# Kernel optimization log

Measured on AMD Instinct MI355X. Metric: run time of the kernel, lower is better.

The kernel has to match this reference:

```python
import jax, jax.numpy as jnp
import numpy as np

B, N, C = 8, 16384, 256
HEADS = 8
TOK = 4  # token_size = (4, 4)


def _unfold3(x):
    # x: (b, c, h, w) -> (b, c, 9, h, w); 3x3 neighborhood, zero padded.
    b, c, h, w = x.shape
    p = jnp.pad(x, ((0, 0), (0, 0), (1, 1), (1, 1)))
    pat = jnp.stack([p[:, :, 1 + dy:1 + dy + h, 1 + dx:1 + dx + w]
                     for dy in (-1, 0, 1) for dx in (-1, 0, 1)], axis=2)
    return pat


def _fold3(u):
    # u: (b, k, 9, h, w) -> (b, k, h, w); scatter-add inverse of _unfold3
    # (matches F.conv_transpose2d with eye(9) kernels, stride 1, pad 1).
    b, k, _, h, w = u.shape
    p = jnp.pad(u, ((0, 0), (0, 0), (0, 0), (1, 1), (1, 1)))
    out = jnp.zeros((b, k, h, w), u.dtype)
    i = 0
    for dy in (-1, 0, 1):
        for dx in (-1, 0, 1):
            out = out + p[:, :, i, 1 - dy:1 - dy + h, 1 - dx:1 - dx + w]
            i += 1
    return out


def setup_inputs() -> dict:
    key = jax.random.key(0)
    k1, k2, k3, k4 = jax.random.split(key, 4)
    x = jax.random.normal(k1, (B, N, C), jnp.float32)
    qkv_w = jax.random.normal(k2, (3 * C, C), jnp.float32) * 0.02
    proj_w = jax.random.normal(k3, (C, C), jnp.float32) * 0.02
    proj_b = jax.random.normal(k4, (C,), jnp.float32) * 0.02
    return {"x": x, "qkv_w": qkv_w, "proj_w": proj_w, "proj_b": proj_b}


def reference(x, qkv_w, proj_w, proj_b):
    b, n, c = x.shape
    H = W = int(np.sqrt(n))
    hh, ww = H // TOK, W // TOK
    nw = hh * ww                      # number of super tokens
    scale = c ** -0.5
    hd = c // HEADS
    head_scale = hd ** -0.5

    xi = jnp.transpose(x, (0, 2, 1)).reshape(b, c, H, W)
    blocks = xi.reshape(b, c, hh, TOK, ww, TOK)
    wf = blocks.mean(axis=(3, 5))                      # (b,c,hh,ww) adaptive avg pool
    pix = blocks.transpose(0, 2, 4, 3, 5, 1).reshape(b, nw, TOK * TOK, c)

    # 3x3 super-token neighborhood features: (b, nw, c, 9)
    wfu = _unfold3(wf).reshape(b, c, 9, nw).transpose(0, 3, 1, 2)

    # pixel <-> super-token affinity, softmax over 9 neighbors
    aff = jax.nn.softmax(jnp.einsum('bnpc,bnck->bnpk', pix, wfu) * scale, axis=-1)

    # normalization: fold of per-window affinity mass -> (b,1,hh,ww)
    aff_sum = _fold3(aff.sum(2).transpose(0, 2, 1).reshape(b, 1, 9, hh, ww))

    # aggregate pixels into super tokens and fold neighborhoods back
    wf2 = jnp.einsum('bnpc,bnpk->bnck', pix, aff)      # (b,nw,c,9)
    wf2 = _fold3(wf2.transpose(0, 2, 3, 1).reshape(b, c, 9, hh, ww))  # (b,c,hh,ww)
    wf2 = wf2 / (jax.lax.stop_gradient(aff_sum) + 1e-12)

    # inner attention over super tokens (non-SDPA: softmax over key axis)
    qkv = jnp.einsum('oc,bchw->bohw', qkv_w, wf2).reshape(b, HEADS, 3 * hd, nw)
    q, k, v = jnp.split(qkv, 3, axis=2)                # each (b,heads,hd,nw)
    attn = jnp.einsum('bhdn,bhdm->bhnm', k, q) * head_scale
    attn = jax.nn.softmax(attn, axis=-2)               # softmax over key index n
    ref = jnp.einsum('bhdn,bhnm->bhdm', v, attn).reshape(b, c, hh, ww)
    ref = jnp.einsum('oc,bchw->bohw', proj_w, ref) + proj_b[None, :, None, None]

    # scatter refined super tokens back to pixels through the affinity
    wfu2 = _unfold3(ref).reshape(b, c, 9, nw).transpose(0, 3, 1, 2)   # (b,nw,c,9)
    pix2 = jnp.einsum('bnck,bnpk->bncp', wfu2, aff)    # (b,nw,c,16)
    pix2 = pix2.reshape(b, hh, ww, c, TOK, TOK).transpose(0, 3, 1, 4, 2, 5)
    pix2 = pix2.reshape(b, c, H, W)
    # NOTE: torch does a raw memory reshape (B,C,H,W)->(B,H*W,C), not a transpose;
    # we replicate that exactly.
    return pix2.reshape(b, H * W, c)
```

## Files before the change

### kernel.cpp

```cpp
#include <hip/hip_runtime.h>

typedef short short8 __attribute__((ext_vector_type(8)));
typedef float f32x4 __attribute__((ext_vector_type(4)));

__device__ __forceinline__ unsigned short f2bf(float x) {
  union { float f; unsigned int u; } v; v.f = x;
  unsigned int r = (v.u + 0x7FFFu + ((v.u >> 16) & 1u)) >> 16;
  return (unsigned short)r;
}
__device__ __forceinline__ float bf2f(unsigned short u) {
  union { unsigned int u; float f; } v; v.u = ((unsigned int)u) << 16;
  return v.f;
}

__global__ __launch_bounds__(256) void k0_wconv(const float* __restrict__ qkvw,
                                                const float* __restrict__ projw,
                                                unsigned short* __restrict__ wqkvbf,
                                                unsigned short* __restrict__ wprojbf) {
  int i = blockIdx.x * 256 + threadIdx.x;
  if (i < 768 * 256) wqkvbf[i] = f2bf(qkvw[i]);
  if (i < 256 * 256) wprojbf[i] = f2bf(projw[i]);
}

__global__ __launch_bounds__(256) void k1_pool(const float* __restrict__ x,
                                               float* __restrict__ wf) {
  int t = threadIdx.x;
  int blk = blockIdx.x;
  int b = blk >> 10, pos = blk & 1023;
  int y = pos >> 5, xw = pos & 31;
  const float* xb = x + (size_t)b * 4194304;
  float acc = 0.f;
  #pragma unroll
  for (int p = 0; p < 16; ++p) {
    int h = 4 * y + (p >> 2), w = 4 * xw + (p & 3);
    acc += xb[(size_t)(h * 128 + w) * 256 + t];
  }
  wf[(size_t)blk * 256 + t] = acc * 0.0625f;
}

__global__ __launch_bounds__(256) void k2_winaff(const float* __restrict__ x,
                                                 const float* __restrict__ wf,
                                                 float* __restrict__ aff_g,
                                                 unsigned short* __restrict__ agg,
                                                 float* __restrict__ asum_w) {
  __shared__ float pixs[16][272];
  __shared__ float wfu[9][272];
  __shared__ float aff_s[16][12];
  int t = threadIdx.x;
  int blk = blockIdx.x;
  int b = blk >> 10, pos = blk & 1023;
  int y = pos >> 5, xw = pos & 31;
  const float* xb = x + (size_t)b * 4194304;

  #pragma unroll
  for (int p = 0; p < 16; ++p) {
    int h = 4 * y + (p >> 2), w = 4 * xw + (p & 3);
    pixs[p][t] = xb[(size_t)(h * 128 + w) * 256 + t];
  }
  #pragma unroll
  for (int i = 0; i < 9; ++i) {
    int dy = i / 3 - 1, dx = i % 3 - 1;
    int ny = y + dy, nx = xw + dx;
    float v = 0.f;
    if (ny >= 0 && ny < 32 && nx >= 0 && nx < 32)
      v = wf[((size_t)(b * 1024) + ny * 32 + nx) * 256 + t];
    wfu[i][t] = v;
  }
  __syncthreads();

  int pp = t >> 4, sub = t & 15;
  #pragma unroll
  for (int i = 0; i < 9; ++i) {
    float acc = 0.f;
    #pragma unroll
    for (int j = 0; j < 16; ++j) acc += pixs[pp][sub + 16 * j] * wfu[i][sub + 16 * j];
    acc += __shfl_xor(acc, 1);
    acc += __shfl_xor(acc, 2);
    acc += __shfl_xor(acc, 4);
    acc += __shfl_xor(acc, 8);
    if (sub == 0) aff_s[pp][i] = acc * 0.0625f;
  }
  __syncthreads();

  if (t < 16) {
    float m = aff_s[t][0];
    #pragma unroll
    for (int i = 1; i < 9; ++i) m = fmaxf(m, aff_s[t][i]);
    float e[9]; float s = 0.f;
    #pragma unroll
    for (int i = 0; i < 9; ++i) { e[i] = __expf(aff_s[t][i] - m); s += e[i]; }
    float inv = 1.f / s;
    #pragma unroll
    for (int i = 0; i < 9; ++i) aff_s[t][i] = e[i] * inv;
  }
  __syncthreads();

  if (t < 144) aff_g[(size_t)blk * 144 + t] = aff_s[t / 9][t % 9];
  if (t < 9) {
    float s = 0.f;
    #pragma unroll
    for (int p = 0; p < 16; ++p) s += aff_s[p][t];
    asum_w[blk * 9 + t] = s;
  }

  #pragma unroll
  for (int k = 0; k < 9; ++k) {
    float acc = 0.f;
    #pragma unroll
    for (int p = 0; p < 16; ++p) acc += pixs[p][t] * aff_s[p][k];
    agg[((size_t)blk * 9 + k) * 256 + t] = f2bf(acc);
  }
}

__global__ __launch_bounds__(256) void k3_gather(const unsigned short* __restrict__ agg,
                                                 const float* __restrict__ asum_w,
                                                 unsigned short* __restrict__ wf2bf) {
  int t = threadIdx.x;
  int blk = blockIdx.x;
  int b = blk >> 10, pos = blk & 1023;
  int y = pos >> 5, xw = pos & 31;
  float acc = 0.f, den = 0.f;
  #pragma unroll
  for (int i = 0; i < 9; ++i) {
    int dy = i / 3 - 1, dx = i % 3 - 1;
    int sy = y - dy, sx = xw - dx;
    if (sy < 0 || sy >= 32 || sx < 0 || sx >= 32) continue;
    size_t un = (size_t)(b * 1024) + sy * 32 + sx;
    acc += bf2f(agg[(un * 9 + i) * 256 + t]);
    den += asum_w[un * 9 + i];
  }
  wf2bf[(size_t)blk * 256 + t] = f2bf(acc / (den + 1e-12f));
}

__global__ __launch_bounds__(256) void k4_qkv(const unsigned short* __restrict__ wbf,
                                              const unsigned short* __restrict__ xbf,
                                              unsigned short* __restrict__ qt,
                                              unsigned short* __restrict__ kt,
                                              unsigned short* __restrict__ vt) {
  int tid = threadIdx.x, lane = tid & 63, wv = tid >> 6;
  int l15 = lane & 15, g = lane >> 4;
  int nb = blockIdx.x * 64 + (wv & 1) * 32;
  int ob = blockIdx.y * 64 + (wv >> 1) * 32;
  int b = blockIdx.z;
  const unsigned short* X = xbf + (size_t)b * 262144;
  f32x4 acc[2][2] = {};
  for (int cc = 0; cc < 256; cc += 32) {
    short8 af[2], bfr[2];
    #pragma unroll
    for (int oi = 0; oi < 2; ++oi)
      af[oi] = *(const short8*)(wbf + (size_t)(ob + oi * 16 + l15) * 256 + cc + g * 8);
    #pragma unroll
    for (int ni = 0; ni < 2; ++ni)
      bfr[ni] = *(const short8*)(X + (size_t)(nb + ni * 16 + l15) * 256 + cc + g * 8);
    #pragma unroll
    for (int oi = 0; oi < 2; ++oi)
      #pragma unroll
      for (int ni = 0; ni < 2; ++ni)
        acc[oi][ni] = __builtin_amdgcn_mfma_f32_16x16x32_bf16(af[oi], bfr[ni], acc[oi][ni], 0, 0, 0);
  }
  #pragma unroll
  for (int oi = 0; oi < 2; ++oi)
    #pragma unroll
    for (int ni = 0; ni < 2; ++ni)
      #pragma unroll
      for (int r = 0; r < 4; ++r) {
        int o = ob + oi * 16 + g * 4 + r;
        int n = nb + ni * 16 + l15;
        unsigned short bv = f2bf(acc[oi][ni][r]);
        int head = o / 96;
        int rr = o - head * 96;
        size_t bh = (size_t)(b * 8 + head);
        if (rr < 32) qt[(bh * 1024 + n) * 32 + rr] = bv;
        else if (rr < 64) kt[(bh * 1024 + n) * 32 + (rr - 32)] = bv;
        else vt[(bh * 32 + (rr - 64)) * 1024 + n] = bv;
      }
}

__global__ __launch_bounds__(256) void k5_attn(const unsigned short* __restrict__ qt,
                                               const unsigned short* __restrict__ kt,
                                               const unsigned short* __restrict__ vt,
                                               unsigned short* __restrict__ refpre) {
  __shared__ short P_lds[4][32][40];
  __shared__ float out_lds[4][32][33];
  __shared__ float den_lds[4][32];
  int tid = threadIdx.x, lane = tid & 63, wv = tid >> 6;
  int l15 = lane & 15, g = lane >> 4;
  int mt = blockIdx.x, h = blockIdx.y, b = blockIdx.z;
  const unsigned short* qtb = qt + ((size_t)(b * 8 + h) * 1024) * 32;
  const unsigned short* ktb = kt + ((size_t)(b * 8 + h) * 1024) * 32;
  const unsigned short* vtb = vt + ((size_t)(b * 8 + h) * 32) * 1024;

  short8 qf[2];
  #pragma unroll
  for (int mi = 0; mi < 2; ++mi) {
    int m = mt * 32 + mi * 16 + l15;
    qf[mi] = *(const short8*)(qtb + (size_t)m * 32 + g * 8);
  }
  f32x4 oacc[2][2] = {};
  float dsum0 = 0.f, dsum1 = 0.f;
  const float hs = 0.17677669529663687f;

  for (int c8 = 0; c8 < 8; ++c8) {
    int nchunk = wv * 256 + c8 * 32;
    f32x4 sf[2][2];
    #pragma unroll
    for (int nt = 0; nt < 2; ++nt) {
      int n = nchunk + nt * 16 + l15;
      short8 kf = *(const short8*)(ktb + (size_t)n * 32 + g * 8);
      #pragma unroll
      for (int mi = 0; mi < 2; ++mi) {
        f32x4 z = {0.f, 0.f, 0.f, 0.f};
        sf[nt][mi] = __builtin_amdgcn_mfma_f32_16x16x32_bf16(kf, qf[mi], z, 0, 0, 0);
      }
    }
    #pragma unroll
    for (int nt = 0; nt < 2; ++nt)
      #pragma unroll
      for (int mi = 0; mi < 2; ++mi) {
        float p0 = __expf(hs * sf[nt][mi][0]);
        float p1 = __expf(hs * sf[nt][mi][1]);
        float p2 = __expf(hs * sf[nt][mi][2]);
        float p3 = __expf(hs * sf[nt][mi][3]);
        float ds = (p0 + p1) + (p2 + p3);
        if (mi == 0) dsum0 += ds; else dsum1 += ds;
        unsigned int w01 = ((unsigned int)f2bf(p1) << 16) | f2bf(p0);
        unsigned int w23 = ((unsigned int)f2bf(p3) << 16) | f2bf(p2);
        int ml = mi * 16 + l15;
        int nn = nt * 16 + g * 4;
        *(unsigned int*)&P_lds[wv][ml][nn] = w01;
        *(unsigned int*)&P_lds[wv][ml][nn + 2] = w23;
      }
    #pragma unroll
    for (int dh = 0; dh < 2; ++dh) {
      short8 vf = *(const short8*)(vtb + (size_t)(dh * 16 + l15) * 1024 + nchunk + g * 8);
      #pragma unroll
      for (int mi = 0; mi < 2; ++mi) {
        short8 pf = *(const short8*)&P_lds[wv][mi * 16 + l15][g * 8];
        oacc[dh][mi] = __builtin_amdgcn_mfma_f32_16x16x32_bf16(vf, pf, oacc[dh][mi], 0, 0, 0);
      }
    }
  }

  dsum0 += __shfl_xor(dsum0, 16); dsum0 += __shfl_xor(dsum0, 32);
  dsum1 += __shfl_xor(dsum1, 16); dsum1 += __shfl_xor(dsum1, 32);
  if (lane < 16) { den_lds[wv][lane] = dsum0; den_lds[wv][16 + lane] = dsum1; }
  #pragma unroll
  for (int dh = 0; dh < 2; ++dh)
    #pragma unroll
    for (int mi = 0; mi < 2; ++mi)
      #pragma unroll
      for (int r = 0; r < 4; ++r)
        out_lds[wv][dh * 16 + g * 4 + r][mi * 16 + l15] = oacc[dh][mi][r];
  __syncthreads();

  #pragma unroll
  for (int kk = 0; kk < 4; ++kk) {
    int idx = kk * 256 + tid;
    int d = idx & 31, m = idx >> 5;
    float v = out_lds[0][d][m] + out_lds[1][d][m] + out_lds[2][d][m] + out_lds[3][d][m];
    float den = den_lds[0][m] + den_lds[1][m] + den_lds[2][m] + den_lds[3][m];
    float res = v / den;
    int n = mt * 32 + m;
    refpre[((size_t)(b * 1024) + n) * 256 + h * 32 + d] = f2bf(res);
  }
}

__global__ __launch_bounds__(256) void k6_proj(const unsigned short* __restrict__ wbf,
                                               const unsigned short* __restrict__ xbf,
                                               const float* __restrict__ bias,
                                               float* __restrict__ reft) {
  int tid = threadIdx.x, lane = tid & 63, wv = tid >> 6;
  int l15 = lane & 15, g = lane >> 4;
  int nb = blockIdx.x * 64 + (wv & 1) * 32;
  int ob = blockIdx.y * 64 + (wv >> 1) * 32;
  int b = blockIdx.z;
  const unsigned short* X = xbf + (size_t)b * 262144;
  f32x4 acc[2][2] = {};
  for (int cc = 0; cc < 256; cc += 32) {
    short8 af[2], bfr[2];
    #pragma unroll
    for (int oi = 0; oi < 2; ++oi)
      af[oi] = *(const short8*)(wbf + (size_t)(ob + oi * 16 + l15) * 256 + cc + g * 8);
    #pragma unroll
    for (int ni = 0; ni < 2; ++ni)
      bfr[ni] = *(const short8*)(X + (size_t)(nb + ni * 16 + l15) * 256 + cc + g * 8);
    #pragma unroll
    for (int oi = 0; oi < 2; ++oi)
      #pragma unroll
      for (int ni = 0; ni < 2; ++ni)
        acc[oi][ni] = __builtin_amdgcn_mfma_f32_16x16x32_bf16(af[oi], bfr[ni], acc[oi][ni], 0, 0, 0);
  }
  #pragma unroll
  for (int oi = 0; oi < 2; ++oi)
    #pragma unroll
    for (int ni = 0; ni < 2; ++ni) {
      int o4 = ob + oi * 16 + g * 4;
      int n = nb + ni * 16 + l15;
      f32x4 b4 = *(const f32x4*)(bias + o4);
      f32x4 r = acc[oi][ni] + b4;
      *(f32x4*)(reft + ((size_t)(b * 1024) + n) * 256 + o4) = r;
    }
}

__global__ __launch_bounds__(256) void k7_scatter(const float* __restrict__ reft,
                                                  const float* __restrict__ aff_g,
                                                  float* __restrict__ out) {
  __shared__ float refn[32 * 3 * 34];
  __shared__ float affl[144 * 33];
  int t = threadIdx.x;
  int cg = blockIdx.x;
  int y = blockIdx.y;
  int b = blockIdx.z;
  int c0 = cg * 32;

  for (int i = t; i < 32 * 3 * 34; i += 256) {
    int c = i & 31;
    int rest = i >> 5;
    int xx = rest % 34;
    int dy = rest / 34;
    int ny = y + dy - 1, nx = xx - 1;
    float v = 0.f;
    if (ny >= 0 && ny < 32 && nx >= 0 && nx < 32)
      v = reft[((size_t)(b * 1024) + ny * 32 + nx) * 256 + c0 + c];
    refn[(c * 3 + dy) * 34 + xx] = v;
  }
  for (int i = t; i < 4608; i += 256) {
    int xw = i / 144;
    int rem = i - xw * 144;
    affl[rem * 33 + xw] = aff_g[((size_t)(b * 1024) + y * 32) * 144 + i];
  }
  __syncthreads();

  for (int kk = 0; kk < 64; ++kk) {
    int idx = kk * 256 + t;
    int wpix = idx & 127;
    int rest = idx >> 7;
    int ii = rest & 3, c = rest >> 2;
    int xw = wpix >> 2, j = wpix & 3;
    int p = ii * 4 + j;
    float acc = 0.f;
    #pragma unroll
    for (int k = 0; k < 9; ++k) {
      int dy = k / 3, kx = k % 3;
      acc += refn[(c * 3 + dy) * 34 + xw + kx] * affl[(p * 9 + k) * 33 + xw];
    }
    out[(size_t)b * 4194304 + (size_t)(c0 + c) * 16384 + (4 * y + ii) * 128 + wpix] = acc;
  }
}

extern "C" void kernel_launch(void* const* d_in, const int* in_sizes, int n_in,
                              void* d_out, int out_size, void* d_ws, size_t ws_size,
                              hipStream_t stream) {
  const float* x = (const float*)d_in[0];
  const float* qkvw = (const float*)d_in[1];
  const float* projw = (const float*)d_in[2];
  const float* projb = (const float*)d_in[3];
  float* out = (float*)d_out;
  char* ws = (char*)d_ws;

  float* wf             = (float*)(ws + 0);
  float* aff            = (float*)(ws + 8388608);
  unsigned short* agg   = (unsigned short*)(ws + 13107200);
  float* asum_w         = (float*)(ws + 50855936);
  unsigned short* wf2bf = (unsigned short*)(ws + 51150848);
  unsigned short* qt    = (unsigned short*)(ws + 55345152);
  unsigned short* kt    = (unsigned short*)(ws + 59539456);
  unsigned short* vt    = (unsigned short*)(ws + 63733760);
  unsigned short* refpre= (unsigned short*)(ws + 67928064);
  float* reft           = (float*)(ws + 72122368);
  unsigned short* wqkvbf = (unsigned short*)(ws + 80510976);
  unsigned short* wprojbf= (unsigned short*)(ws + 80904192);

  k0_wconv<<<768, 256, 0, stream>>>(qkvw, projw, wqkvbf, wprojbf);
  k1_pool<<<8192, 256, 0, stream>>>(x, wf);
  k2_winaff<<<8192, 256, 0, stream>>>(x, wf, aff, agg, asum_w);
  k3_gather<<<8192, 256, 0, stream>>>(agg, asum_w, wf2bf);
  k4_qkv<<<dim3(16, 12, 8), 256, 0, stream>>>(wqkvbf, wf2bf, qt, kt, vt);
  k5_attn<<<dim3(32, 8, 8), 256, 0, stream>>>(qt, kt, vt, refpre);
  k6_proj<<<dim3(16, 4, 8), 256, 0, stream>>>(wprojbf, refpre, projb, reft);
  k7_scatter<<<dim3(8, 32, 8), 256, 0, stream>>>(reft, aff, out);
}
```

Measured before the change: 414.6 us.

## Compute pixel-supertoken affinity with bf16 MFMA, one wave per window

The window-affinity kernel now assigns one wavefront per super-token window and computes the 16x9 pixel/neighbor logits with a bf16 MFMA instead of scalar FP32 dot products through shared memory. The pooled features are stored as bf16 and pixel inputs are truncated to bf16 in registers. Softmax is done with cross-lane shuffles. Affinities are written directly in the padded transposed layout that the scatter kernel reads, so its load becomes a straight copy. This cuts LDS traffic and block syncs, at the cost of reduced precision in the softmax logits (truncation, not rounding, for pixel values).

```diff
diff --git a/kernel.cpp b/kernel.cpp
--- a/kernel.cpp
+++ b/kernel.cpp
@@ -2,6 +2,7 @@
 
 typedef short short8 __attribute__((ext_vector_type(8)));
 typedef float f32x4 __attribute__((ext_vector_type(4)));
+typedef unsigned int uint2v __attribute__((ext_vector_type(2)));
 
 __device__ __forceinline__ unsigned short f2bf(float x) {
   union { float f; unsigned int u; } v; v.f = x;
@@ -23,7 +24,7 @@
 }
 
 __global__ __launch_bounds__(256) void k1_pool(const float* __restrict__ x,
-                                               float* __restrict__ wf) {
+                                               unsigned short* __restrict__ wfbf) {
   int t = threadIdx.x;
   int blk = blockIdx.x;
   int b = blk >> 10, pos = blk & 1023;
@@ -35,80 +36,100 @@
     int h = 4 * y + (p >> 2), w = 4 * xw + (p & 3);
     acc += xb[(size_t)(h * 128 + w) * 256 + t];
   }
-  wf[(size_t)blk * 256 + t] = acc * 0.0625f;
+  wfbf[(size_t)blk * 256 + t] = f2bf(acc * 0.0625f);
 }
 
 __global__ __launch_bounds__(256) void k2_winaff(const float* __restrict__ x,
-                                                 const float* __restrict__ wf,
-                                                 float* __restrict__ aff_g,
+                                                 const unsigned short* __restrict__ wfbf,
+                                                 float* __restrict__ aff2,
                                                  unsigned short* __restrict__ agg,
                                                  float* __restrict__ asum_w) {
-  __shared__ float pixs[16][272];
-  __shared__ float wfu[9][272];
-  __shared__ float aff_s[16][12];
-  int t = threadIdx.x;
-  int blk = blockIdx.x;
-  int b = blk >> 10, pos = blk & 1023;
+  __shared__ float aff_lds[4][16][16];
+  int tid = threadIdx.x, wv = tid >> 6, lane = tid & 63;
+  int l15 = lane & 15, g = lane >> 4;
+  int u = blockIdx.x * 4 + wv;
+  int b = u >> 10, pos = u & 1023;
   int y = pos >> 5, xw = pos & 31;
   const float* xb = x + (size_t)b * 4194304;
 
+  int dyi = l15 / 3 - 1, dxi = (l15 % 3) - 1;
+  bool valid_n = (l15 < 9) && ((unsigned)(y + dyi) < 32u) && ((unsigned)(xw + dxi) < 32u);
+  int un = valid_n ? (b * 1024 + (y + dyi) * 32 + (xw + dxi)) : 0;
+  const unsigned short* wrow = wfbf + (size_t)un * 256;
+
+  int ph = 4 * y + (l15 >> 2), pw = 4 * xw + (l15 & 3);
+  const float* prow = xb + (size_t)(ph * 128 + pw) * 256;
+
+  const short8 zero8 = {0, 0, 0, 0, 0, 0, 0, 0};
+  f32x4 S = {0.f, 0.f, 0.f, 0.f};
+  #pragma unroll
+  for (int cc = 0; cc < 256; cc += 32) {
+    short8 af = *(const short8*)(wrow + cc + g * 8);
+    af = valid_n ? af : zero8;
+    f32x4 lo = *(const f32x4*)(prow + cc + g * 8);
+    f32x4 hi = *(const f32x4*)(prow + cc + g * 8 + 4);
+    union { unsigned int w[4]; f32x4 f; } L, H;
+    L.f = lo; H.f = hi;
+    union { unsigned int w[4]; short8 s; } cv;
+    cv.w[0] = (L.w[1] & 0xFFFF0000u) | (L.w[0] >> 16);
+    cv.w[1] = (L.w[3] & 0xFFFF0000u) | (L.w[2] >> 16);
+    cv.w[2] = (H.w[1] & 0xFFFF0000u) | (H.w[0] >> 16);
+    cv.w[3] = (H.w[3] & 0xFFFF0000u) | (H.w[2] >> 16);
+    S = __builtin_amdgcn_mfma_f32_16x16x32_bf16(af, cv.s, S, 0, 0, 0);
+  }
+
+  const float scale = 0.0625f;
+  float Lg[4], e4[4];
+  float pmax = -1e30f;
+  #pragma unroll
+  for (int r = 0; r < 4; ++r) {
+    Lg[r] = S[r] * scale;
+    bool v = (g * 4 + r) < 9;
+    pmax = v ? fmaxf(pmax, Lg[r]) : pmax;
+  }
+  pmax = fmaxf(pmax, __shfl_xor(pmax, 16));
+  pmax = fmaxf(pmax, __shfl_xor(pmax, 32));
+  float esum = 0.f;
+  #pragma unroll
+  for (int r = 0; r < 4; ++r) {
+    bool v = (g * 4 + r) < 9;
+    e4[r] = v ? __expf(Lg[r] - pmax) : 0.f;
+    esum += e4[r];
+  }
+  esum += __shfl_xor(esum, 16);
+  esum += __shfl_xor(esum, 32);
+  float inv = 1.f / esum;
+  int rowbase = (b * 32 + y) * 4752;
+  #pragma unroll
+  for (int r = 0; r < 4; ++r) {
+    float a = e4[r] * inv;
+    aff_lds[wv][g * 4 + r][l15] = a;
+    float s = a;
+    s += __shfl_xor(s, 1); s += __shfl_xor(s, 2);
+    s += __shfl_xor(s, 4); s += __shfl_xor(s, 8);
+    if ((g * 4 + r) < 9) {
+      aff2[rowbase + (l15 * 9 + g * 4 + r) * 33 + xw] = a;
+      if (l15 == 0) asum_w[u * 9 + g * 4 + r] = s;
+    }
+  }
+
+  f32x4 acc[9] = {};
   #pragma unroll
   for (int p = 0; p < 16; ++p) {
-    int h = 4 * y + (p >> 2), w = 4 * xw + (p & 3);
-    pixs[p][t] = xb[(size_t)(h * 128 + w) * 256 + t];
-  }
-  #pragma unroll
-  for (int i = 0; i < 9; ++i) {
-    int dy = i / 3 - 1, dx = i % 3 - 1;
-    int ny = y + dy, nx = xw + dx;
-    float v = 0.f;
-    if (ny >= 0 && ny < 32 && nx >= 0 && nx < 32)
-      v = wf[((size_t)(b * 1024) + ny * 32 + nx) * 256 + t];
-    wfu[i][t] = v;
-  }
-  __syncthreads();
-
-  int pp = t >> 4, sub = t & 15;
-  #pragma unroll
-  for (int i = 0; i < 9; ++i) {
-    float acc = 0.f;
-    #pragma unroll
-    for (int j = 0; j < 16; ++j) acc += pixs[pp][sub + 16 * j] * wfu[i][sub + 16 * j];
-    acc += __shfl_xor(acc, 1);
-    acc += __shfl_xor(acc, 2);
-    acc += __shfl_xor(acc, 4);
-    acc += __shfl_xor(acc, 8);
-    if (sub == 0) aff_s[pp][i] = acc * 0.0625f;
-  }
-  __syncthreads();
-
-  if (t < 16) {
-    float m = aff_s[t][0];
-    #pragma unroll
-    for (int i = 1; i < 9; ++i) m = fmaxf(m, aff_s[t][i]);
-    float e[9]; float s = 0.f;
-    #pragma unroll
-    for (int i = 0; i < 9; ++i) { e[i] = __expf(aff_s[t][i] - m); s += e[i]; }
-    float inv = 1.f / s;
-    #pragma unroll
-    for (int i = 0; i < 9; ++i) aff_s[t][i] = e[i] * inv;
-  }
-  __syncthreads();
-
-  if (t < 144) aff_g[(size_t)blk * 144 + t] = aff_s[t / 9][t % 9];
-  if (t < 9) {
-    float s = 0.f;
-    #pragma unroll
-    for (int p = 0; p < 16; ++p) s += aff_s[p][t];
-    asum_w[blk * 9 + t] = s;
-  }
-
+    int phh = 4 * y + (p >> 2), pww = 4 * xw + (p & 3);
+    f32x4 pf = *(const f32x4*)(xb + (size_t)(phh * 128 + pww) * 256 + 4 * lane);
+    #pragma unroll
+    for (int k = 0; k < 9; ++k) {
+      float ab = aff_lds[wv][k][p];
+      acc[k] += ab * pf;
+    }
+  }
   #pragma unroll
   for (int k = 0; k < 9; ++k) {
-    float acc = 0.f;
-    #pragma unroll
-    for (int p = 0; p < 16; ++p) acc += pixs[p][t] * aff_s[p][k];
-    agg[((size_t)blk * 9 + k) * 256 + t] = f2bf(acc);
+    uint2v st;
+    st.x = ((unsigned int)f2bf(acc[k][1]) << 16) | f2bf(acc[k][0]);
+    st.y = ((unsigned int)f2bf(acc[k][3]) << 16) | f2bf(acc[k][2]);
+    *(uint2v*)(agg + ((size_t)u * 9 + k) * 256 + 4 * lane) = st;
   }
 }
 
@@ -303,7 +324,7 @@
 }
 
 __global__ __launch_bounds__(256) void k7_scatter(const float* __restrict__ reft,
-                                                  const float* __restrict__ aff_g,
+                                                  const float* __restrict__ aff2,
                                                   float* __restrict__ out) {
   __shared__ float refn[32 * 3 * 34];
   __shared__ float affl[144 * 33];
@@ -324,10 +345,9 @@
       v = reft[((size_t)(b * 1024) + ny * 32 + nx) * 256 + c0 + c];
     refn[(c * 3 + dy) * 34 + xx] = v;
   }
-  for (int i = t; i < 4608; i += 256) {
-    int xw = i / 144;
-    int rem = i - xw * 144;
-    affl[rem * 33 + xw] = aff_g[((size_t)(b * 1024) + y * 32) * 144 + i];
+  int abase = (b * 32 + y) * 4752;
+  for (int i = t; i < 4752; i += 256) {
+    affl[i] = aff2[abase + i];
   }
   __syncthreads();
 
@@ -358,25 +378,25 @@
   float* out = (float*)d_out;
   char* ws = (char*)d_ws;
 
-  float* wf             = (float*)(ws + 0);
-  float* aff            = (float*)(ws + 8388608);
-  unsigned short* agg   = (unsigned short*)(ws + 13107200);
-  float* asum_w         = (float*)(ws + 50855936);
-  unsigned short* wf2bf = (unsigned short*)(ws + 51150848);
-  unsigned short* qt    = (unsigned short*)(ws + 55345152);
-  unsigned short* kt    = (unsigned short*)(ws + 59539456);
-  unsigned short* vt    = (unsigned short*)(ws + 63733760);
-  unsigned short* refpre= (unsigned short*)(ws + 67928064);
-  float* reft           = (float*)(ws + 72122368);
-  unsigned short* wqkvbf = (unsigned short*)(ws + 80510976);
-  unsigned short* wprojbf= (unsigned short*)(ws + 80904192);
+  unsigned short* wfbf   = (unsigned short*)(ws + 0);
+  float* aff2            = (float*)(ws + 4194304);
+  unsigned short* agg    = (unsigned short*)(ws + 9060352);
+  float* asum_w          = (float*)(ws + 46809088);
+  unsigned short* wf2bf  = (unsigned short*)(ws + 47104000);
+  unsigned short* qt     = (unsigned short*)(ws + 51298304);
+  unsigned short* kt     = (unsigned short*)(ws + 55492608);
+  unsigned short* vt     = (unsigned short*)(ws + 59686912);
+  unsigned short* refpre = (unsigned short*)(ws + 63881216);
+  float* reft            = (float*)(ws + 68075520);
+  unsigned short* wqkvbf = (unsigned short*)(ws + 76464128);
+  unsigned short* wprojbf= (unsigned short*)(ws + 76857344);
 
   k0_wconv<<<768, 256, 0, stream>>>(qkvw, projw, wqkvbf, wprojbf);
-  k1_pool<<<8192, 256, 0, stream>>>(x, wf);
-  k2_winaff<<<8192, 256, 0, stream>>>(x, wf, aff, agg, asum_w);
+  k1_pool<<<8192, 256, 0, stream>>>(x, wfbf);
+  k2_winaff<<<2048, 256, 0, stream>>>(x, wfbf, aff2, agg, asum_w);
   k3_gather<<<8192, 256, 0, stream>>>(agg, asum_w, wf2bf);
   k4_qkv<<<dim3(16, 12, 8), 256, 0, stream>>>(wqkvbf, wf2bf, qt, kt, vt);
   k5_attn<<<dim3(32, 8, 8), 256, 0, stream>>>(qt, kt, vt, refpre);
   k6_proj<<<dim3(16, 4, 8), 256, 0, stream>>>(wprojbf, refpre, projb, reft);
-  k7_scatter<<<dim3(8, 32, 8), 256, 0, stream>>>(reft, aff, out);
-}
+  k7_scatter<<<dim3(8, 32, 8), 256, 0, stream>>>(reft, aff2, out);
+}
```

Result: faster. 388.9 us (-6.2%).
